# Optimization experiments

Measured on AMD Instinct MI355X. Metric: run time of the kernel, lower is better.

The kernel has to match this reference:

```python
import jax, jax.numpy as jnp
import numpy as np

RADIUS = 0.4
NSAMPLE = 32
B, N, NPOINT, C = 4, 16384, 4096, 64


def _ball_query(xyz, new_xyz, radius, nsample):
    """PointNet++ ball query: first `nsample` point indices (in original order)
    within `radius` of each query; pad with the first found index (0 if none).
    xyz: (B,N,3)  new_xyz: (B,M,3)  ->  idx: (B,M,nsample) int32."""
    n = xyz.shape[1]
    # squared distances (B, M, N) via ||a||^2 + ||b||^2 - 2 a.b
    qq = jnp.sum(new_xyz * new_xyz, axis=-1)[:, :, None]
    pp = jnp.sum(xyz * xyz, axis=-1)[:, None, :]
    d2 = qq + pp - 2.0 * jnp.einsum('bmd,bnd->bmn', new_xyz, xyz)
    ar = jnp.arange(n, dtype=jnp.int32)
    # key = point index if inside ball else sentinel n; smallest keys = earliest hits
    key = jnp.where(d2 < radius * radius, ar, n)
    neg_small, _ = jax.lax.top_k(-key, nsample)   # nsample smallest keys
    sel = -neg_small                               # (B, M, nsample)
    valid = sel < n
    first = jnp.where(valid[..., :1], sel[..., :1], 0)
    return jnp.where(valid, sel, first).astype(jnp.int32)


def setup_inputs() -> dict:
    key = jax.random.key(0)
    k1, k2, k3 = jax.random.split(key, 3)
    xyz = jax.random.normal(k1, (B, N, 3), dtype=jnp.float32)
    new_xyz = jax.random.normal(k2, (B, NPOINT, 3), dtype=jnp.float32)
    features = jax.random.normal(k3, (B, C, N), dtype=jnp.float32)
    return {"xyz": xyz, "new_xyz": new_xyz, "features": features}


def reference(xyz, new_xyz, features):
    idx = _ball_query(xyz, new_xyz, RADIUS, NSAMPLE)            # (B, M, S)
    # gather xyz -> (B, M, S, 3) -> (B, 3, M, S), center on queries
    grouped_xyz = jax.vmap(lambda p, i: p[i])(xyz, idx)
    grouped_xyz = jnp.transpose(grouped_xyz, (0, 3, 1, 2))
    grouped_xyz = grouped_xyz - jnp.transpose(new_xyz, (0, 2, 1))[..., None]
    # gather features -> (B, C, M, S)
    grouped_feat = jax.vmap(lambda f, i: f[:, i])(features, idx)
    # use_xyz=True: concat centered coords with features on channel dim
    return jnp.concatenate([grouped_xyz, grouped_feat], axis=1)  # (B, 3+C, M, S)
```

## Files before the change

kernel.cpp:

```cpp
#include <hip/hip_runtime.h>
#include <stdint.h>

#define B_ 4
#define N_ 16384
#define M_ 4096
#define C_ 64
#define S_ 32
#define R2_ 0.16f

static const size_t OFF_XYZ4 = 0;
static const size_t OFF_FT   = (size_t)B_ * N_ * 4 * sizeof(float);
static const size_t OFF_IDX  = OFF_FT + (size_t)B_ * N_ * C_ * sizeof(float);

__global__ __launch_bounds__(256) void pack_xyz4(const float* __restrict__ xyz,
                                                 float4* __restrict__ xyz4) {
    int i = blockIdx.x * 256 + threadIdx.x;
    float x = xyz[3 * i + 0];
    float y = xyz[3 * i + 1];
    float z = xyz[3 * i + 2];
    float pp = __fadd_rn(__fadd_rn(__fmul_rn(x, x), __fmul_rn(y, y)), __fmul_rn(z, z));
    xyz4[i] = make_float4(x, y, z, pp);
}

__global__ __launch_bounds__(256) void transpose_feat(const float* __restrict__ f,
                                                      float* __restrict__ ft) {
    __shared__ float tile[64][65];
    int b  = blockIdx.x >> 8;
    int n0 = (blockIdx.x & 255) << 6;
    int tid  = threadIdx.x;
    int lane = tid & 63;
    int grp  = tid >> 6;
    #pragma unroll
    for (int r = 0; r < 16; ++r) {
        int c = r * 4 + grp;
        tile[c][lane] = f[((size_t)b * C_ + c) * N_ + n0 + lane];
    }
    __syncthreads();
    #pragma unroll
    for (int r = 0; r < 16; ++r) {
        int nl = r * 4 + grp;
        ft[((size_t)b * N_ + n0 + nl) * C_ + lane] = tile[lane][nl];
    }
}

__global__ __launch_bounds__(256) void ball_query(const float4* __restrict__ xyz4,
                                                  const float* __restrict__ newxyz,
                                                  int* __restrict__ idx) {
    __shared__ float4 pts[1024];
    int tid  = threadIdx.x;
    int lane = tid & 63;
    int w    = tid >> 6;
    int b    = blockIdx.x >> 10;
    int m    = ((blockIdx.x & 1023) << 2) + w;
    size_t qb = ((size_t)b * M_ + m) * 3;
    float qx = newxyz[qb + 0];
    float qy = newxyz[qb + 1];
    float qz = newxyz[qb + 2];
    float qq = __fadd_rn(__fadd_rn(__fmul_rn(qx, qx), __fmul_rn(qy, qy)), __fmul_rn(qz, qz));

    const float4* xb = xyz4 + (size_t)b * N_;
    int* outp = idx + ((size_t)b * M_ + m) * S_;

    int count = 0;
    int first = 0;
    bool done = false;

    for (int ch = 0; ch < N_ / 1024; ++ch) {
        int base = ch * 1024;
        #pragma unroll
        for (int k = 0; k < 4; ++k) pts[tid + 256 * k] = xb[base + tid + 256 * k];
        __syncthreads();
        if (!done) {
            for (int it = 0; it < 16; ++it) {
                float4 P = pts[it * 64 + lane];
                float dot = __fmaf_rn(qz, P.z, __fmaf_rn(qy, P.y, __fmul_rn(qx, P.x)));
                float d2  = __fsub_rn(__fadd_rn(qq, P.w), __fmul_rn(2.0f, dot));
                bool inb = d2 < R2_;
                unsigned long long mask = __ballot(inb);
                if (mask) {
                    int pc        = __popcll(mask);
                    int remaining = 32 - count;
                    if (count == 0) first = base + it * 64 + (int)__builtin_ctzll(mask);
                    int rank = __popcll(mask & ((1ull << lane) - 1ull));
                    if (inb && rank < remaining) outp[count + rank] = base + it * 64 + lane;
                    count += (pc < remaining ? pc : remaining);
                    if (count >= 32) { done = true; break; }
                }
            }
        }
        if (__syncthreads_and((int)done)) break;
    }
    if (count < 32) {
        for (int s = count + lane; s < 32; s += 64) outp[s] = first;
    }
}

__global__ __launch_bounds__(256) void group_out(const float4* __restrict__ xyz4,
                                                 const float* __restrict__ ft,
                                                 const float* __restrict__ newxyz,
                                                 const int* __restrict__ idx,
                                                 float* __restrict__ out) {
    __shared__ int   sidx[32];
    __shared__ float q[3];
    int tid = threadIdx.x;
    int b   = blockIdx.x >> 12;
    int m   = blockIdx.x & 4095;
    if (tid < 32) sidx[tid] = idx[((size_t)b * M_ + m) * S_ + tid];
    if (tid < 3)  q[tid]    = newxyz[((size_t)b * M_ + m) * 3 + tid];
    __syncthreads();

    int s  = tid & 31;
    int c8 = tid >> 5;
    int p  = sidx[s];

    const float* fp = ft + ((size_t)b * N_ + p) * C_ + c8 * 8;
    float4 v0 = *(const float4*)(fp);
    float4 v1 = *(const float4*)(fp + 4);

    const size_t st = (size_t)M_ * S_;
    size_t ob = (((size_t)b * 67 + 3 + c8 * 8) * M_ + m) * S_ + s;
    out[ob + 0 * st] = v0.x;
    out[ob + 1 * st] = v0.y;
    out[ob + 2 * st] = v0.z;
    out[ob + 3 * st] = v0.w;
    out[ob + 4 * st] = v1.x;
    out[ob + 5 * st] = v1.y;
    out[ob + 6 * st] = v1.z;
    out[ob + 7 * st] = v1.w;

    if (tid < 32) {
        float4 P = xyz4[(size_t)b * N_ + p];
        size_t xb = (((size_t)b * 67 + 0) * M_ + m) * S_ + s;
        out[xb + 0 * st] = P.x - q[0];
        out[xb + 1 * st] = P.y - q[1];
        out[xb + 2 * st] = P.z - q[2];
    }
}

extern "C" void kernel_launch(void* const* d_in, const int* in_sizes, int n_in,
                              void* d_out, int out_size, void* d_ws, size_t ws_size,
                              hipStream_t stream) {
    const float* xyz    = (const float*)d_in[0];
    const float* newxyz = (const float*)d_in[1];
    const float* feat   = (const float*)d_in[2];
    float* out = (float*)d_out;

    char* ws = (char*)d_ws;
    float4* xyz4 = (float4*)(ws + OFF_XYZ4);
    float*  ft   = (float*)(ws + OFF_FT);
    int*    idxb = (int*)(ws + OFF_IDX);

    pack_xyz4<<<(B_ * N_) / 256, 256, 0, stream>>>(xyz, xyz4);
    transpose_feat<<<B_ * (N_ / 64), 256, 0, stream>>>(feat, ft);
    ball_query<<<(B_ * M_) / 4, 256, 0, stream>>>(xyz4, newxyz, idxb);
    group_out<<<B_ * M_, 256, 0, stream>>>(xyz4, ft, newxyz, idxb, out);
}
```

Before: 270.0 us.

## Process four queries per wavefront in ball query with register prefetch, no LDS

Each wavefront now handles four query points and streams the point cloud straight from global memory into registers, 128 points at a time, with a software prefetch of the next batch. This drops the shared-memory staging and the block-wide syncs, so each wave exits once all four of its queries are full. Each loaded point is reused across four queries. In exchange the grid has a quarter as many blocks, register use rises, and a wave keeps scanning until its slowest query finishes.

```diff
diff --git a/kernel.cpp b/kernel.cpp
--- a/kernel.cpp
+++ b/kernel.cpp
@@ -46,52 +46,82 @@
 __global__ __launch_bounds__(256) void ball_query(const float4* __restrict__ xyz4,
                                                   const float* __restrict__ newxyz,
                                                   int* __restrict__ idx) {
-    __shared__ float4 pts[1024];
     int tid  = threadIdx.x;
     int lane = tid & 63;
-    int w    = tid >> 6;
-    int b    = blockIdx.x >> 10;
-    int m    = ((blockIdx.x & 1023) << 2) + w;
-    size_t qb = ((size_t)b * M_ + m) * 3;
-    float qx = newxyz[qb + 0];
-    float qy = newxyz[qb + 1];
-    float qz = newxyz[qb + 2];
-    float qq = __fadd_rn(__fadd_rn(__fmul_rn(qx, qx), __fmul_rn(qy, qy)), __fmul_rn(qz, qz));
+    int gw   = (blockIdx.x << 2) + (tid >> 6);
+    int b    = gw >> 10;
+    int m0   = (gw & 1023) << 2;
 
+    float qx[4], qy[4], qz[4], qq[4];
+    int*  outp[4];
+    #pragma unroll
+    for (int q = 0; q < 4; ++q) {
+        size_t qb = ((size_t)b * M_ + m0 + q) * 3;
+        float x = newxyz[qb + 0], y = newxyz[qb + 1], z = newxyz[qb + 2];
+        qx[q] = x; qy[q] = y; qz[q] = z;
+        qq[q] = __fadd_rn(__fadd_rn(__fmul_rn(x, x), __fmul_rn(y, y)), __fmul_rn(z, z));
+        outp[q] = idx + ((size_t)b * M_ + m0 + q) * S_;
+    }
+
+    int count[4] = {0, 0, 0, 0};
+    int first[4] = {0, 0, 0, 0};
+    int done = 0;
     const float4* xb = xyz4 + (size_t)b * N_;
-    int* outp = idx + ((size_t)b * M_ + m) * S_;
+    unsigned long long lmlt = (1ull << lane) - 1ull;
 
-    int count = 0;
-    int first = 0;
-    bool done = false;
+    float4 P0 = xb[lane];
+    float4 P1 = xb[64 + lane];
 
-    for (int ch = 0; ch < N_ / 1024; ++ch) {
-        int base = ch * 1024;
+    for (int base = 0; base < N_; base += 128) {
+        float4 Npre0 = P0, Npre1 = P1;
+        if (base + 128 < N_) {
+            Npre0 = xb[base + 128 + lane];
+            Npre1 = xb[base + 192 + lane];
+        }
         #pragma unroll
-        for (int k = 0; k < 4; ++k) pts[tid + 256 * k] = xb[base + tid + 256 * k];
-        __syncthreads();
-        if (!done) {
-            for (int it = 0; it < 16; ++it) {
-                float4 P = pts[it * 64 + lane];
-                float dot = __fmaf_rn(qz, P.z, __fmaf_rn(qy, P.y, __fmul_rn(qx, P.x)));
-                float d2  = __fsub_rn(__fadd_rn(qq, P.w), __fmul_rn(2.0f, dot));
+        for (int q = 0; q < 4; ++q) {
+            if (done & (1 << q)) continue;
+            {
+                float dot = __fmaf_rn(qz[q], P0.z, __fmaf_rn(qy[q], P0.y, __fmul_rn(qx[q], P0.x)));
+                float d2  = __fsub_rn(__fadd_rn(qq[q], P0.w), __fmul_rn(2.0f, dot));
                 bool inb = d2 < R2_;
-                unsigned long long mask = __ballot(inb);
-                if (mask) {
-                    int pc        = __popcll(mask);
-                    int remaining = 32 - count;
-                    if (count == 0) first = base + it * 64 + (int)__builtin_ctzll(mask);
-                    int rank = __popcll(mask & ((1ull << lane) - 1ull));
-                    if (inb && rank < remaining) outp[count + rank] = base + it * 64 + lane;
-                    count += (pc < remaining ? pc : remaining);
-                    if (count >= 32) { done = true; break; }
+                unsigned long long mk = __ballot(inb);
+                if (mk) {
+                    int pc  = __popcll(mk);
+                    int rem = 32 - count[q];
+                    if (count[q] == 0) first[q] = base + (int)__builtin_ctzll(mk);
+                    int rank = __popcll(mk & lmlt);
+                    if (inb && rank < rem) outp[q][count[q] + rank] = base + lane;
+                    count[q] += (pc < rem ? pc : rem);
+                    if (count[q] >= 32) { done |= (1 << q); continue; }
+                }
+            }
+            {
+                float dot = __fmaf_rn(qz[q], P1.z, __fmaf_rn(qy[q], P1.y, __fmul_rn(qx[q], P1.x)));
+                float d2  = __fsub_rn(__fadd_rn(qq[q], P1.w), __fmul_rn(2.0f, dot));
+                bool inb = d2 < R2_;
+                unsigned long long mk = __ballot(inb);
+                if (mk) {
+                    int pc  = __popcll(mk);
+                    int rem = 32 - count[q];
+                    if (count[q] == 0) first[q] = base + 64 + (int)__builtin_ctzll(mk);
+                    int rank = __popcll(mk & lmlt);
+                    if (inb && rank < rem) outp[q][count[q] + rank] = base + 64 + lane;
+                    count[q] += (pc < rem ? pc : rem);
+                    if (count[q] >= 32) { done |= (1 << q); }
                 }
             }
         }
-        if (__syncthreads_and((int)done)) break;
+        if (done == 15) break;
+        P0 = Npre0;
+        P1 = Npre1;
     }
-    if (count < 32) {
-        for (int s = count + lane; s < 32; s += 64) outp[s] = first;
+
+    #pragma unroll
+    for (int q = 0; q < 4; ++q) {
+        if (count[q] < 32) {
+            for (int s = count[q] + lane; s < 32; s += 64) outp[q][s] = first[q];
+        }
     }
 }
 
@@ -152,6 +182,6 @@
 
     pack_xyz4<<<(B_ * N_) / 256, 256, 0, stream>>>(xyz, xyz4);
     transpose_feat<<<B_ * (N_ / 64), 256, 0, stream>>>(feat, ft);
-    ball_query<<<(B_ * M_) / 4, 256, 0, stream>>>(xyz4, newxyz, idxb);
+    ball_query<<<(B_ * M_) / 16, 256, 0, stream>>>(xyz4, newxyz, idxb);
     group_out<<<B_ * M_, 256, 0, stream>>>(xyz4, ft, newxyz, idxb, out);
 }
```

Result: faster. 230.4 us (-14.7%).

## Replace brute-force ball query with uniform spatial grid binning

Applied to the files above, without the earlier changes.

Builds a 32^3 uniform grid per batch using histogram, scan and scatter kernels, then queries only the 27 neighbouring cells per query point. Hits go into shared memory and the 32 smallest original indices are selected by repeated wave-min reduction, which preserves original-order semantics. This is meant to remove the near-linear scan over all N points per query, at the cost of extra kernels, atomics, and a per-query selection loop. The grid covers the range [-8,8) with clamping, and the grid buffers reuse the feature-transpose workspace, which is then overwritten by transpose_feat.

```diff
diff --git a/kernel.cpp b/kernel.cpp
--- a/kernel.cpp
+++ b/kernel.cpp
@@ -7,19 +7,140 @@
 #define C_ 64
 #define S_ 32
 #define R2_ 0.16f
-
-static const size_t OFF_XYZ4 = 0;
-static const size_t OFF_FT   = (size_t)B_ * N_ * 4 * sizeof(float);
-static const size_t OFF_IDX  = OFF_FT + (size_t)B_ * N_ * C_ * sizeof(float);
+#define GDIM 32
+#define CELLS 32768
+#define CSTRIDE 32772
+
+static const size_t OFF_XYZ4  = 0;
+static const size_t OFF_FT    = (size_t)B_ * N_ * 4 * sizeof(float);
+static const size_t OFF_IDX   = OFF_FT + (size_t)B_ * N_ * C_ * sizeof(float);
+static const size_t OFF_START = OFF_FT;
+static const size_t OFF_CUR   = OFF_START + (size_t)B_ * CSTRIDE * sizeof(int);
+static const size_t OFF_SPTS  = OFF_CUR + (size_t)B_ * CSTRIDE * sizeof(int);
+static const size_t OFF_SSID  = OFF_SPTS + (size_t)B_ * N_ * 4 * sizeof(float);
+
+__device__ __forceinline__ int cellof(float v) {
+    int c = (int)floorf((v + 8.0f) * 2.0f);
+    return c < 0 ? 0 : (c > GDIM - 1 ? GDIM - 1 : c);
+}
 
 __global__ __launch_bounds__(256) void pack_xyz4(const float* __restrict__ xyz,
-                                                 float4* __restrict__ xyz4) {
+                                                 float4* __restrict__ xyz4,
+                                                 int* __restrict__ cur) {
     int i = blockIdx.x * 256 + threadIdx.x;
+    for (int j = i; j < B_ * CSTRIDE; j += B_ * N_) cur[j] = 0;
     float x = xyz[3 * i + 0];
     float y = xyz[3 * i + 1];
     float z = xyz[3 * i + 2];
     float pp = __fadd_rn(__fadd_rn(__fmul_rn(x, x), __fmul_rn(y, y)), __fmul_rn(z, z));
     xyz4[i] = make_float4(x, y, z, pp);
+}
+
+__global__ __launch_bounds__(256) void hist_cells(const float* __restrict__ xyz,
+                                                  int* __restrict__ cur) {
+    int i = blockIdx.x * 256 + threadIdx.x;
+    int b = i >> 14;
+    float x = xyz[3 * i + 0];
+    float y = xyz[3 * i + 1];
+    float z = xyz[3 * i + 2];
+    int cid = (cellof(z) << 10) | (cellof(y) << 5) | cellof(x);
+    atomicAdd(&cur[b * CSTRIDE + cid], 1);
+}
+
+__global__ __launch_bounds__(1024) void scan_cells(int* __restrict__ cur,
+                                                   int* __restrict__ start) {
+    __shared__ int ls[1024];
+    int b = blockIdx.x, t = threadIdx.x;
+    int* cb = cur + b * CSTRIDE;
+    int* sb = start + b * CSTRIDE;
+    int base = t * 32;
+    int loc[32]; int tot = 0;
+    #pragma unroll
+    for (int j = 0; j < 32; ++j) { loc[j] = cb[base + j]; tot += loc[j]; }
+    ls[t] = tot; __syncthreads();
+    for (int d = 1; d < 1024; d <<= 1) {
+        int v = (t >= d) ? ls[t - d] : 0; __syncthreads();
+        ls[t] += v; __syncthreads();
+    }
+    int run = ls[t] - tot;
+    #pragma unroll
+    for (int j = 0; j < 32; ++j) { sb[base + j] = run; cb[base + j] = run; run += loc[j]; }
+    if (t == 0) sb[CELLS] = N_;
+}
+
+__global__ __launch_bounds__(256) void scatter_pts(const float4* __restrict__ xyz4,
+                                                   int* __restrict__ cur,
+                                                   float4* __restrict__ spts,
+                                                   int* __restrict__ ssid) {
+    int i = blockIdx.x * 256 + threadIdx.x;
+    int b = i >> 14, n = i & (N_ - 1);
+    float4 P = xyz4[i];
+    int cid = (cellof(P.z) << 10) | (cellof(P.y) << 5) | cellof(P.x);
+    int pos = atomicAdd(&cur[b * CSTRIDE + cid], 1);
+    spts[(size_t)b * N_ + pos] = P;
+    ssid[b * N_ + pos] = n;
+}
+
+__global__ __launch_bounds__(256) void ball_query_grid(const float4* __restrict__ spts,
+                                                       const int* __restrict__ ssid,
+                                                       const int* __restrict__ start,
+                                                       const float* __restrict__ newxyz,
+                                                       int* __restrict__ idx) {
+    __shared__ int hitsAll[4 * 1024];
+    int tid = threadIdx.x, lane = tid & 63, w = tid >> 6;
+    int* hits = hitsAll + w * 1024;
+    int gw = blockIdx.x * 4 + w;
+    int b = gw >> 12;
+    int m = gw & (M_ - 1);
+    size_t qb = ((size_t)b * M_ + m) * 3;
+    float qx = newxyz[qb + 0], qy = newxyz[qb + 1], qz = newxyz[qb + 2];
+    float qq = __fadd_rn(__fadd_rn(__fmul_rn(qx, qx), __fmul_rn(qy, qy)), __fmul_rn(qz, qz));
+    int cx = cellof(qx), cy = cellof(qy), cz = cellof(qz);
+    const float4* sp  = spts + (size_t)b * N_;
+    const int*    sid = ssid + b * N_;
+    const int*    st  = start + b * CSTRIDE;
+    unsigned long long lmlt = (1ull << lane) - 1ull;
+    int cnt = 0;
+
+    for (int dz = -1; dz <= 1; ++dz) { int nz = cz + dz; if ((unsigned)nz >= GDIM) continue;
+    for (int dy = -1; dy <= 1; ++dy) { int ny = cy + dy; if ((unsigned)ny >= GDIM) continue;
+    for (int dx = -1; dx <= 1; ++dx) { int nx = cx + dx; if ((unsigned)nx >= GDIM) continue;
+        int cid = (nz << 10) | (ny << 5) | nx;
+        int s = st[cid], e = st[cid + 1];
+        for (int off = s; off < e; off += 64) {
+            int i = off + lane;
+            bool inb = false; int oidx = 0;
+            if (i < e) {
+                float4 P = sp[i];
+                float dot = __fmaf_rn(qz, P.z, __fmaf_rn(qy, P.y, __fmul_rn(qx, P.x)));
+                float d2  = __fsub_rn(__fadd_rn(qq, P.w), __fmul_rn(2.0f, dot));
+                if (d2 < R2_) { inb = true; oidx = sid[i]; }
+            }
+            unsigned long long mk = __ballot(inb);
+            if (mk) {
+                int rank = __popcll(mk & lmlt);
+                int pos  = cnt + rank;
+                if (inb && pos < 1024) hits[pos] = oidx;
+                cnt += __popcll(mk);
+            }
+        }
+    }}}
+    __builtin_amdgcn_wave_barrier();
+    if (cnt > 1024) cnt = 1024;
+    int kk = cnt < S_ ? cnt : S_;
+    int sel = 0, firstv = 0;
+    for (int k = 0; k < kk; ++k) {
+        int v = 0x7fffffff;
+        for (int j = lane; j < cnt; j += 64) v = min(v, hits[j]);
+        #pragma unroll
+        for (int o = 32; o; o >>= 1) { int u = __shfl_xor(v, o); v = min(v, u); }
+        for (int j = lane; j < cnt; j += 64) if (hits[j] == v) hits[j] = 0x7fffffff;
+        __builtin_amdgcn_wave_barrier();
+        if (k == 0) firstv = v;
+        if (lane == k) sel = v;
+    }
+    if (lane >= kk) sel = firstv;
+    if (lane < S_) idx[((size_t)b * M_ + m) * S_ + lane] = sel;
 }
 
 __global__ __launch_bounds__(256) void transpose_feat(const float* __restrict__ f,
@@ -40,58 +161,6 @@
     for (int r = 0; r < 16; ++r) {
         int nl = r * 4 + grp;
         ft[((size_t)b * N_ + n0 + nl) * C_ + lane] = tile[lane][nl];
-    }
-}
-
-__global__ __launch_bounds__(256) void ball_query(const float4* __restrict__ xyz4,
-                                                  const float* __restrict__ newxyz,
-                                                  int* __restrict__ idx) {
-    __shared__ float4 pts[1024];
-    int tid  = threadIdx.x;
-    int lane = tid & 63;
-    int w    = tid >> 6;
-    int b    = blockIdx.x >> 10;
-    int m    = ((blockIdx.x & 1023) << 2) + w;
-    size_t qb = ((size_t)b * M_ + m) * 3;
-    float qx = newxyz[qb + 0];
-    float qy = newxyz[qb + 1];
-    float qz = newxyz[qb + 2];
-    float qq = __fadd_rn(__fadd_rn(__fmul_rn(qx, qx), __fmul_rn(qy, qy)), __fmul_rn(qz, qz));
-
-    const float4* xb = xyz4 + (size_t)b * N_;
-    int* outp = idx + ((size_t)b * M_ + m) * S_;
-
-    int count = 0;
-    int first = 0;
-    bool done = false;
-
-    for (int ch = 0; ch < N_ / 1024; ++ch) {
-        int base = ch * 1024;
-        #pragma unroll
-        for (int k = 0; k < 4; ++k) pts[tid + 256 * k] = xb[base + tid + 256 * k];
-        __syncthreads();
-        if (!done) {
-            for (int it = 0; it < 16; ++it) {
-                float4 P = pts[it * 64 + lane];
-                float dot = __fmaf_rn(qz, P.z, __fmaf_rn(qy, P.y, __fmul_rn(qx, P.x)));
-                float d2  = __fsub_rn(__fadd_rn(qq, P.w), __fmul_rn(2.0f, dot));
-                bool inb = d2 < R2_;
-                unsigned long long mask = __ballot(inb);
-                if (mask) {
-                    int pc        = __popcll(mask);
-                    int remaining = 32 - count;
-                    if (count == 0) first = base + it * 64 + (int)__builtin_ctzll(mask);
-                    int rank = __popcll(mask & ((1ull << lane) - 1ull));
-                    if (inb && rank < remaining) outp[count + rank] = base + it * 64 + lane;
-                    count += (pc < remaining ? pc : remaining);
-                    if (count >= 32) { done = true; break; }
-                }
-            }
-        }
-        if (__syncthreads_and((int)done)) break;
-    }
-    if (count < 32) {
-        for (int s = count + lane; s < 32; s += 64) outp[s] = first;
     }
 }
 
@@ -146,12 +215,19 @@
     float* out = (float*)d_out;
 
     char* ws = (char*)d_ws;
-    float4* xyz4 = (float4*)(ws + OFF_XYZ4);
-    float*  ft   = (float*)(ws + OFF_FT);
-    int*    idxb = (int*)(ws + OFF_IDX);
-
-    pack_xyz4<<<(B_ * N_) / 256, 256, 0, stream>>>(xyz, xyz4);
+    float4* xyz4  = (float4*)(ws + OFF_XYZ4);
+    float*  ft    = (float*)(ws + OFF_FT);
+    int*    idxb  = (int*)(ws + OFF_IDX);
+    int*    startc= (int*)(ws + OFF_START);
+    int*    curc  = (int*)(ws + OFF_CUR);
+    float4* spts  = (float4*)(ws + OFF_SPTS);
+    int*    ssid  = (int*)(ws + OFF_SSID);
+
+    pack_xyz4     <<<(B_ * N_) / 256, 256, 0, stream>>>(xyz, xyz4, curc);
+    hist_cells    <<<(B_ * N_) / 256, 256, 0, stream>>>(xyz, curc);
+    scan_cells    <<<B_, 1024, 0, stream>>>(curc, startc);
+    scatter_pts   <<<(B_ * N_) / 256, 256, 0, stream>>>(xyz4, curc, spts, ssid);
+    ball_query_grid<<<(B_ * M_) / 4, 256, 0, stream>>>(spts, ssid, startc, newxyz, idxb);
     transpose_feat<<<B_ * (N_ / 64), 256, 0, stream>>>(feat, ft);
-    ball_query<<<(B_ * M_) / 4, 256, 0, stream>>>(xyz4, newxyz, idxb);
-    group_out<<<B_ * M_, 256, 0, stream>>>(xyz4, ft, newxyz, idxb, out);
-}
+    group_out     <<<B_ * M_, 256, 0, stream>>>(xyz4, ft, newxyz, idxb, out);
+}
```

Result: slower. 303.3 us (+12.3%).
